# Optimization experiments

Measured on AMD Instinct MI355X. Metric: run time of the kernel, lower is better.

## Reference

```python
import jax, jax.numpy as jnp
import numpy as np
import math


def setup_inputs() -> dict:
    key = jax.random.key(0)
    kq, kk, kv = jax.random.split(key, 3)
    B, H, S, D = 8, 12, 4096, 64
    q = jax.random.normal(kq, (B, H, S, D), dtype=jnp.float32)
    k = jax.random.normal(kk, (B, H, S, D), dtype=jnp.float32)
    v = jax.random.normal(kv, (B, H, S, D), dtype=jnp.float32)
    return {"q": q, "k": k, "v": v}


def reference(q, k, v):
    B, H, S, D = q.shape
    topk = int(2 * math.sqrt(S))  # 128 for S=4096
    # importance = mean + std (torch.std is unbiased -> ddof=1)
    importance = q.mean(axis=-1) + jnp.std(q, axis=-1, ddof=1)  # [B,H,S]
    _, idx = jax.lax.top_k(importance, topk)  # [B,H,topk]
    idx_e = idx[..., None]  # [B,H,topk,1]
    q_s = jnp.take_along_axis(q, idx_e, axis=2)  # [B,H,topk,D]
    k_s = jnp.take_along_axis(k, idx_e, axis=2)
    v_s = jnp.take_along_axis(v, idx_e, axis=2)
    scores = jnp.einsum('bhtd,bhsd->bhts', q_s, k_s) / math.sqrt(D)
    attn = jax.nn.softmax(scores, axis=-1)
    out_s = jnp.einsum('bhts,bhsd->bhtd', attn, v_s)  # [B,H,topk,D]
    # scatter back into a full tensor (torch uses empty_like; we use zeros
    # for the unselected positions so the output is deterministic)
    bI = jnp.arange(B)[:, None, None]
    hI = jnp.arange(H)[None, :, None]
    out = jnp.zeros_like(v).at[bI, hI, idx].set(out_s)  # [B,H,S,D]
    Himg = int(math.sqrt(S))
    return out.reshape(B, -1, Himg, Himg)  # [B, H*D, Himg, Himg]
```

## Files before the change

kernel.cpp:

```cpp
#include <hip/hip_runtime.h>
#include <hip/hip_fp16.h>
#include <math.h>

#define BH_N 96
#define S_N 4096
#define D_N 64
#define TOPK 128

__device__ __forceinline__ unsigned long long orderKey(double d) {
  unsigned long long u = (unsigned long long)__double_as_longlong(d);
  if (u & 0x8000000000000000ULL) u = ~u;
  else u |= 0x8000000000000000ULL;
  return u;
}

__global__ __launch_bounds__(256)
void imp_zero_kernel(const float* __restrict__ q, float* __restrict__ out,
                     double* __restrict__ imp) {
  const int tid = threadIdx.x;
  const size_t off = (size_t)blockIdx.x * 1024 + (size_t)tid * 4;
  const float4 v = *reinterpret_cast<const float4*>(q + off);
  float4 z; z.x = z.y = z.z = z.w = 0.f;
  *reinterpret_cast<float4*>(out + off) = z;

  double s  = (double)v.x + (double)v.y + (double)v.z + (double)v.w;
  double ss = (double)v.x * v.x + (double)v.y * v.y +
              (double)v.z * v.z + (double)v.w * v.w;
#pragma unroll
  for (int m = 1; m < 16; m <<= 1) {
    s  += __shfl_xor(s, m, 64);
    ss += __shfl_xor(ss, m, 64);
  }
  if ((tid & 15) == 0) {
    double mean = s * (1.0 / 64.0);
    double var = (ss - s * s * (1.0 / 64.0)) * (1.0 / 63.0);
    if (var < 0.0) var = 0.0;
    imp[(size_t)blockIdx.x * 16 + (tid >> 4)] = mean + sqrt(var);
  }
}

__global__ __launch_bounds__(256)
void topk_attn_kernel(const float* __restrict__ q, const float* __restrict__ k,
                      const float* __restrict__ v, const double* __restrict__ imp,
                      float* __restrict__ out) {
  __shared__ __align__(16) float sA[8448];
  __shared__ __align__(16) float sB[4160];
  __shared__ int s_idx[TOPK];
  __shared__ int s_red[4];
  __shared__ int s_cnt;

  const int tid = threadIdx.x;
  const int lane = tid & 63;
  const int wv = tid >> 6;
  const int bh = blockIdx.x;
  const double* impb = imp + (size_t)bh * S_N;

  unsigned long long key[16];
#pragma unroll
  for (int i = 0; i < 16; ++i) key[i] = orderKey(impb[i * 256 + tid]);

  unsigned long long lo = 0ULL, hi = ~0ULL;
  while (lo < hi) {
    unsigned long long d = hi - lo;
    unsigned long long mid = lo + (d >> 1) + (d & 1ULL);
    int c = 0;
#pragma unroll
    for (int i = 0; i < 16; ++i) c += (key[i] >= mid) ? 1 : 0;
#pragma unroll
    for (int m = 1; m < 64; m <<= 1) c += __shfl_xor(c, m, 64);
    if (lane == 0) s_red[wv] = c;
    __syncthreads();
    int total = s_red[0] + s_red[1] + s_red[2] + s_red[3];
    __syncthreads();
    if (total >= TOPK) lo = mid; else hi = mid - 1;
  }
  const unsigned long long T = lo;

  if (tid == 0) s_cnt = 0;
  __syncthreads();
#pragma unroll
  for (int i = 0; i < 16; ++i) {
    if (key[i] > T) {
      int slot = atomicAdd(&s_cnt, 1);
      s_idx[slot] = i * 256 + tid;
    }
  }
  __syncthreads();
  const int nsel = s_cnt;
  const int need = TOPK - nsel;
  if (wv == 0 && need > 0) {
    int running = 0;
    for (int base = 0; base < S_N && running < need; base += 64) {
      unsigned long long kk2 = orderKey(impb[base + lane]);
      unsigned long long mask = __ballot(kk2 == T);
      if (kk2 == T) {
        int below = __popcll(mask & ((1ULL << lane) - 1ULL));
        int pos = running + below;
        if (pos < need) s_idx[nsel + pos] = base + lane;
      }
      running += __popcll(mask);
    }
  }
  __syncthreads();

  const size_t baseQ = (size_t)bh * S_N * D_N;
  const int rgrp = tid >> 4;
  const int c4 = (tid & 15) * 4;

#pragma unroll
  for (int it = 0; it < 8; ++it) {
    int r = it * 16 + rgrp;
    int srow = s_idx[r];
    float4 val = *reinterpret_cast<const float4*>(q + baseQ + (size_t)srow * D_N + c4);
    sA[r * 65 + c4 + 0] = val.x;
    sA[r * 65 + c4 + 1] = val.y;
    sA[r * 65 + c4 + 2] = val.z;
    sA[r * 65 + c4 + 3] = val.w;
  }

  float acc[8][8];
#pragma unroll
  for (int j = 0; j < 8; ++j)
#pragma unroll
    for (int m = 0; m < 8; ++m) acc[j][m] = 0.f;

  const int tq = tid >> 4;
  const int sq = tid & 15;

  for (int h = 0; h < 2; ++h) {
    __syncthreads();
#pragma unroll
    for (int it = 0; it < 4; ++it) {
      int r = it * 16 + rgrp;
      int srow = s_idx[h * 64 + r];
      float4 val = *reinterpret_cast<const float4*>(k + baseQ + (size_t)srow * D_N + c4);
      sB[r * 65 + c4 + 0] = val.x;
      sB[r * 65 + c4 + 1] = val.y;
      sB[r * 65 + c4 + 2] = val.z;
      sB[r * 65 + c4 + 3] = val.w;
    }
    __syncthreads();
    for (int kk = 0; kk < 64; ++kk) {
      float qv[8], kv[4];
#pragma unroll
      for (int j = 0; j < 8; ++j) qv[j] = sA[(8 * tq + j) * 65 + kk];
#pragma unroll
      for (int m = 0; m < 4; ++m) kv[m] = sB[(4 * sq + m) * 65 + kk];
#pragma unroll
      for (int j = 0; j < 8; ++j)
#pragma unroll
        for (int m = 0; m < 4; ++m) acc[j][h * 4 + m] += qv[j] * kv[m];
    }
  }
  __syncthreads();

  __half* sP = reinterpret_cast<__half*>(sA);
  float rmax[8], rsum[8];
#pragma unroll
  for (int j = 0; j < 8; ++j) {
    float mx = acc[j][0];
#pragma unroll
    for (int m = 1; m < 8; ++m) mx = fmaxf(mx, acc[j][m]);
    rmax[j] = mx;
  }
#pragma unroll
  for (int mm = 1; mm < 16; mm <<= 1)
#pragma unroll
    for (int j = 0; j < 8; ++j) rmax[j] = fmaxf(rmax[j], __shfl_xor(rmax[j], mm, 64));
#pragma unroll
  for (int j = 0; j < 8; ++j) {
    float sum = 0.f;
#pragma unroll
    for (int m = 0; m < 8; ++m) {
      float p = __expf(0.125f * (acc[j][m] - rmax[j]));
      acc[j][m] = p;
      sum += p;
    }
    rsum[j] = sum;
  }
#pragma unroll
  for (int mm = 1; mm < 16; mm <<= 1)
#pragma unroll
    for (int j = 0; j < 8; ++j) rsum[j] += __shfl_xor(rsum[j], mm, 64);
#pragma unroll
  for (int j = 0; j < 8; ++j) {
    float rinv = 1.f / rsum[j];
#pragma unroll
    for (int h2 = 0; h2 < 2; ++h2)
#pragma unroll
      for (int m = 0; m < 4; ++m) {
        int col = h2 * 64 + 4 * sq + m;
        sP[(8 * tq + j) * 132 + col] = __float2half_rn(acc[j][h2 * 4 + m] * rinv);
      }
  }

  float acc2[8][4];
#pragma unroll
  for (int j = 0; j < 8; ++j)
#pragma unroll
    for (int m = 0; m < 4; ++m) acc2[j][m] = 0.f;

  const int ti = tq, di = sq;
  for (int h = 0; h < 2; ++h) {
    __syncthreads();
#pragma unroll
    for (int it = 0; it < 4; ++it) {
      int r = it * 16 + rgrp;
      int srow = s_idx[h * 64 + r];
      float4 val = *reinterpret_cast<const float4*>(v + baseQ + (size_t)srow * D_N + c4);
      sB[r * 65 + c4 + 0] = val.x;
      sB[r * 65 + c4 + 1] = val.y;
      sB[r * 65 + c4 + 2] = val.z;
      sB[r * 65 + c4 + 3] = val.w;
    }
    __syncthreads();
    for (int s2 = 0; s2 < 64; ++s2) {
      int scol = h * 64 + s2;
      float pj[8], vm[4];
#pragma unroll
      for (int j = 0; j < 8; ++j) pj[j] = __half2float(sP[(8 * ti + j) * 132 + scol]);
#pragma unroll
      for (int m = 0; m < 4; ++m) vm[m] = sB[s2 * 65 + 4 * di + m];
#pragma unroll
      for (int j = 0; j < 8; ++j)
#pragma unroll
        for (int m = 0; m < 4; ++m) acc2[j][m] += pj[j] * vm[m];
    }
  }

#pragma unroll
  for (int j = 0; j < 8; ++j) {
    int row = 8 * ti + j;
    int srow = s_idx[row];
    float4 val;
    val.x = acc2[j][0]; val.y = acc2[j][1]; val.z = acc2[j][2]; val.w = acc2[j][3];
    *reinterpret_cast<float4*>(out + baseQ + (size_t)srow * D_N + 4 * di) = val;
  }
}

extern "C" void kernel_launch(void* const* d_in, const int* in_sizes, int n_in,
                              void* d_out, int out_size, void* d_ws, size_t ws_size,
                              hipStream_t stream) {
  const float* q = (const float*)d_in[0];
  const float* k = (const float*)d_in[1];
  const float* v = (const float*)d_in[2];
  float* out = (float*)d_out;
  double* imp = (double*)d_ws;

  imp_zero_kernel<<<24576, 256, 0, stream>>>(q, out, imp);
  topk_attn_kernel<<<BH_N, 256, 0, stream>>>(q, k, v, imp, out);
}
```

Before: 318.4 us.

## Split top-k selection and attention into separate kernels with more parallelism

```diff
diff --git a/kernel.cpp b/kernel.cpp
--- a/kernel.cpp
+++ b/kernel.cpp
@@ -7,8 +7,10 @@
 #define D_N 64
 #define TOPK 128
 
-__device__ __forceinline__ unsigned long long orderKey(double d) {
-  unsigned long long u = (unsigned long long)__double_as_longlong(d);
+typedef unsigned long long ull;
+
+__device__ __forceinline__ ull orderKey(double d) {
+  ull u = (ull)__double_as_longlong(d);
   if (u & 0x8000000000000000ULL) u = ~u;
   else u |= 0x8000000000000000ULL;
   return u;
@@ -16,7 +18,7 @@
 
 __global__ __launch_bounds__(256)
 void imp_zero_kernel(const float* __restrict__ q, float* __restrict__ out,
-                     double* __restrict__ imp) {
+                     ull* __restrict__ keys) {
   const int tid = threadIdx.x;
   const size_t off = (size_t)blockIdx.x * 1024 + (size_t)tid * 4;
   const float4 v = *reinterpret_cast<const float4*>(q + off);
@@ -35,97 +37,112 @@
     double mean = s * (1.0 / 64.0);
     double var = (ss - s * s * (1.0 / 64.0)) * (1.0 / 63.0);
     if (var < 0.0) var = 0.0;
-    imp[(size_t)blockIdx.x * 16 + (tid >> 4)] = mean + sqrt(var);
-  }
-}
-
-__global__ __launch_bounds__(256)
-void topk_attn_kernel(const float* __restrict__ q, const float* __restrict__ k,
-                      const float* __restrict__ v, const double* __restrict__ imp,
-                      float* __restrict__ out) {
-  __shared__ __align__(16) float sA[8448];
-  __shared__ __align__(16) float sB[4160];
+    keys[(size_t)blockIdx.x * 16 + (tid >> 4)] = orderKey(mean + sqrt(var));
+  }
+}
+
+__global__ __launch_bounds__(1024)
+void sel_kernel(const ull* __restrict__ keys, int* __restrict__ idx_out) {
+  __shared__ int red[2][16];
   __shared__ int s_idx[TOPK];
-  __shared__ int s_red[4];
-  __shared__ int s_cnt;
+  __shared__ int s_tidx[1024];
+  __shared__ int s_cnt, s_tcnt;
 
   const int tid = threadIdx.x;
   const int lane = tid & 63;
   const int wv = tid >> 6;
   const int bh = blockIdx.x;
-  const double* impb = imp + (size_t)bh * S_N;
-
-  unsigned long long key[16];
-#pragma unroll
-  for (int i = 0; i < 16; ++i) key[i] = orderKey(impb[i * 256 + tid]);
-
-  unsigned long long lo = 0ULL, hi = ~0ULL;
+  const ull* kb = keys + (size_t)bh * S_N;
+
+  ull key[4];
+#pragma unroll
+  for (int i = 0; i < 4; ++i) key[i] = kb[i * 1024 + tid];
+
+  if (tid == 0) { s_cnt = 0; s_tcnt = 0; }
+
+  ull lo = 0ULL, hi = ~0ULL;
+  int p = 0;
   while (lo < hi) {
-    unsigned long long d = hi - lo;
-    unsigned long long mid = lo + (d >> 1) + (d & 1ULL);
+    ull d = hi - lo;
+    ull mid = lo + (d >> 1) + (d & 1ULL);
     int c = 0;
 #pragma unroll
-    for (int i = 0; i < 16; ++i) c += (key[i] >= mid) ? 1 : 0;
-#pragma unroll
-    for (int m = 1; m < 64; m <<= 1) c += __shfl_xor(c, m, 64);
-    if (lane == 0) s_red[wv] = c;
-    __syncthreads();
-    int total = s_red[0] + s_red[1] + s_red[2] + s_red[3];
-    __syncthreads();
+    for (int i = 0; i < 4; ++i) c += __popcll(__ballot(key[i] >= mid));
+    if (lane == 0) red[p][wv] = c;
+    __syncthreads();
+    int total = 0;
+#pragma unroll
+    for (int w = 0; w < 16; ++w) total += red[p][w];
     if (total >= TOPK) lo = mid; else hi = mid - 1;
-  }
-  const unsigned long long T = lo;
-
-  if (tid == 0) s_cnt = 0;
-  __syncthreads();
-#pragma unroll
-  for (int i = 0; i < 16; ++i) {
+    p ^= 1;
+  }
+  const ull T = lo;
+
+#pragma unroll
+  for (int i = 0; i < 4; ++i) {
     if (key[i] > T) {
       int slot = atomicAdd(&s_cnt, 1);
-      s_idx[slot] = i * 256 + tid;
+      s_idx[slot] = i * 1024 + tid;
+    } else if (key[i] == T) {
+      int sl = atomicAdd(&s_tcnt, 1);
+      if (sl < 1024) s_tidx[sl] = i * 1024 + tid;
     }
   }
   __syncthreads();
   const int nsel = s_cnt;
   const int need = TOPK - nsel;
   if (wv == 0 && need > 0) {
-    int running = 0;
-    for (int base = 0; base < S_N && running < need; base += 64) {
-      unsigned long long kk2 = orderKey(impb[base + lane]);
-      unsigned long long mask = __ballot(kk2 == T);
-      if (kk2 == T) {
-        int below = __popcll(mask & ((1ULL << lane) - 1ULL));
-        int pos = running + below;
-        if (pos < need) s_idx[nsel + pos] = base + lane;
-      }
-      running += __popcll(mask);
+    int t = s_tcnt < 1024 ? s_tcnt : 1024;
+    for (int sel = 0; sel < need; ++sel) {
+      int mymin = 0x7fffffff;
+      for (int j = lane; j < t; j += 64) mymin = min(mymin, s_tidx[j]);
+#pragma unroll
+      for (int m = 1; m < 64; m <<= 1) mymin = min(mymin, __shfl_xor(mymin, m, 64));
+      if (lane == 0) s_idx[nsel + sel] = mymin;
+      for (int j = lane; j < t; j += 64)
+        if (s_tidx[j] == mymin) s_tidx[j] = 0x7fffffff;
     }
   }
   __syncthreads();
-
-  const size_t baseQ = (size_t)bh * S_N * D_N;
+  if (tid < TOPK) idx_out[bh * TOPK + tid] = s_idx[tid];
+}
+
+__global__ __launch_bounds__(256)
+void attn_kernel(const float* __restrict__ q, const float* __restrict__ k,
+                 const float* __restrict__ v, const int* __restrict__ idx_all,
+                 float* __restrict__ out) {
+  __shared__ __align__(16) float sQ[32 * 65];
+  __shared__ __align__(16) float sB[64 * 65];
+  __shared__ __align__(16) __half sP[32 * 132];
+  __shared__ int s_idx[TOPK];
+
+  const int tid = threadIdx.x;
+  const int bh = blockIdx.x >> 2;
+  const int sub = blockIdx.x & 3;
+  if (tid < TOPK) s_idx[tid] = idx_all[bh * TOPK + tid];
+
+  const size_t base = (size_t)bh * S_N * D_N;
   const int rgrp = tid >> 4;
   const int c4 = (tid & 15) * 4;
-
-#pragma unroll
-  for (int it = 0; it < 8; ++it) {
+  const int rr = tid >> 4;
+  const int cc = tid & 15;
+
+  __syncthreads();
+
+#pragma unroll
+  for (int it = 0; it < 2; ++it) {
     int r = it * 16 + rgrp;
-    int srow = s_idx[r];
-    float4 val = *reinterpret_cast<const float4*>(q + baseQ + (size_t)srow * D_N + c4);
-    sA[r * 65 + c4 + 0] = val.x;
-    sA[r * 65 + c4 + 1] = val.y;
-    sA[r * 65 + c4 + 2] = val.z;
-    sA[r * 65 + c4 + 3] = val.w;
-  }
-
-  float acc[8][8];
-#pragma unroll
-  for (int j = 0; j < 8; ++j)
+    int srow = s_idx[sub * 32 + r];
+    float4 val = *reinterpret_cast<const float4*>(q + base + (size_t)srow * D_N + c4);
+    sQ[r * 65 + c4 + 0] = val.x; sQ[r * 65 + c4 + 1] = val.y;
+    sQ[r * 65 + c4 + 2] = val.z; sQ[r * 65 + c4 + 3] = val.w;
+  }
+
+  float acc[2][8];
+#pragma unroll
+  for (int j = 0; j < 2; ++j)
 #pragma unroll
     for (int m = 0; m < 8; ++m) acc[j][m] = 0.f;
-
-  const int tq = tid >> 4;
-  const int sq = tid & 15;
 
   for (int h = 0; h < 2; ++h) {
     __syncthreads();
@@ -133,31 +150,31 @@
     for (int it = 0; it < 4; ++it) {
       int r = it * 16 + rgrp;
       int srow = s_idx[h * 64 + r];
-      float4 val = *reinterpret_cast<const float4*>(k + baseQ + (size_t)srow * D_N + c4);
-      sB[r * 65 + c4 + 0] = val.x;
-      sB[r * 65 + c4 + 1] = val.y;
-      sB[r * 65 + c4 + 2] = val.z;
-      sB[r * 65 + c4 + 3] = val.w;
-    }
-    __syncthreads();
-    for (int kk = 0; kk < 64; ++kk) {
-      float qv[8], kv[4];
-#pragma unroll
-      for (int j = 0; j < 8; ++j) qv[j] = sA[(8 * tq + j) * 65 + kk];
-#pragma unroll
-      for (int m = 0; m < 4; ++m) kv[m] = sB[(4 * sq + m) * 65 + kk];
-#pragma unroll
-      for (int j = 0; j < 8; ++j)
-#pragma unroll
-        for (int m = 0; m < 4; ++m) acc[j][h * 4 + m] += qv[j] * kv[m];
-    }
-  }
-  __syncthreads();
-
-  __half* sP = reinterpret_cast<__half*>(sA);
-  float rmax[8], rsum[8];
-#pragma unroll
-  for (int j = 0; j < 8; ++j) {
+      float4 val = *reinterpret_cast<const float4*>(k + base + (size_t)srow * D_N + c4);
+      sB[r * 65 + c4 + 0] = val.x; sB[r * 65 + c4 + 1] = val.y;
+      sB[r * 65 + c4 + 2] = val.z; sB[r * 65 + c4 + 3] = val.w;
+    }
+    __syncthreads();
+    for (int kk = 0; kk < 64; kk += 2) {
+#pragma unroll
+      for (int u = 0; u < 2; ++u) {
+        float qv0 = sQ[(2 * rr + 0) * 65 + kk + u];
+        float qv1 = sQ[(2 * rr + 1) * 65 + kk + u];
+        float kv[4];
+#pragma unroll
+        for (int m = 0; m < 4; ++m) kv[m] = sB[(cc * 4 + m) * 65 + kk + u];
+#pragma unroll
+        for (int m = 0; m < 4; ++m) {
+          acc[0][h * 4 + m] += qv0 * kv[m];
+          acc[1][h * 4 + m] += qv1 * kv[m];
+        }
+      }
+    }
+  }
+
+  float rmax[2], rsum[2];
+#pragma unroll
+  for (int j = 0; j < 2; ++j) {
     float mx = acc[j][0];
 #pragma unroll
     for (int m = 1; m < 8; ++m) mx = fmaxf(mx, acc[j][m]);
@@ -166,75 +183,72 @@
 #pragma unroll
   for (int mm = 1; mm < 16; mm <<= 1)
 #pragma unroll
-    for (int j = 0; j < 8; ++j) rmax[j] = fmaxf(rmax[j], __shfl_xor(rmax[j], mm, 64));
-#pragma unroll
-  for (int j = 0; j < 8; ++j) {
+    for (int j = 0; j < 2; ++j) rmax[j] = fmaxf(rmax[j], __shfl_xor(rmax[j], mm, 64));
+#pragma unroll
+  for (int j = 0; j < 2; ++j) {
     float sum = 0.f;
 #pragma unroll
     for (int m = 0; m < 8; ++m) {
-      float p = __expf(0.125f * (acc[j][m] - rmax[j]));
-      acc[j][m] = p;
-      sum += p;
+      float pe = __expf(0.125f * (acc[j][m] - rmax[j]));
+      acc[j][m] = pe;
+      sum += pe;
     }
     rsum[j] = sum;
   }
 #pragma unroll
   for (int mm = 1; mm < 16; mm <<= 1)
 #pragma unroll
-    for (int j = 0; j < 8; ++j) rsum[j] += __shfl_xor(rsum[j], mm, 64);
-#pragma unroll
-  for (int j = 0; j < 8; ++j) {
+    for (int j = 0; j < 2; ++j) rsum[j] += __shfl_xor(rsum[j], mm, 64);
+#pragma unroll
+  for (int j = 0; j < 2; ++j) {
     float rinv = 1.f / rsum[j];
 #pragma unroll
     for (int h2 = 0; h2 < 2; ++h2)
 #pragma unroll
       for (int m = 0; m < 4; ++m) {
-        int col = h2 * 64 + 4 * sq + m;
-        sP[(8 * tq + j) * 132 + col] = __float2half_rn(acc[j][h2 * 4 + m] * rinv);
+        int col = h2 * 64 + cc * 4 + m;
+        sP[(2 * rr + j) * 132 + col] = __float2half_rn(acc[j][h2 * 4 + m] * rinv);
       }
   }
 
-  float acc2[8][4];
-#pragma unroll
-  for (int j = 0; j < 8; ++j)
+  float acc2[2][4];
+#pragma unroll
+  for (int j = 0; j < 2; ++j)
 #pragma unroll
     for (int m = 0; m < 4; ++m) acc2[j][m] = 0.f;
 
-  const int ti = tq, di = sq;
   for (int h = 0; h < 2; ++h) {
     __syncthreads();
 #pragma unroll
     for (int it = 0; it < 4; ++it) {
       int r = it * 16 + rgrp;
       int srow = s_idx[h * 64 + r];
-      float4 val = *reinterpret_cast<const float4*>(v + baseQ + (size_t)srow * D_N + c4);
-      sB[r * 65 + c4 + 0] = val.x;
-      sB[r * 65 + c4 + 1] = val.y;
-      sB[r * 65 + c4 + 2] = val.z;
-      sB[r * 65 + c4 + 3] = val.w;
+      float4 val = *reinterpret_cast<const float4*>(v + base + (size_t)srow * D_N + c4);
+      sB[r * 65 + c4 + 0] = val.x; sB[r * 65 + c4 + 1] = val.y;
+      sB[r * 65 + c4 + 2] = val.z; sB[r * 65 + c4 + 3] = val.w;
     }
     __syncthreads();
     for (int s2 = 0; s2 < 64; ++s2) {
       int scol = h * 64 + s2;
-      float pj[8], vm[4];
-#pragma unroll
-      for (int j = 0; j < 8; ++j) pj[j] = __half2float(sP[(8 * ti + j) * 132 + scol]);
-#pragma unroll
-      for (int m = 0; m < 4; ++m) vm[m] = sB[s2 * 65 + 4 * di + m];
-#pragma unroll
-      for (int j = 0; j < 8; ++j)
-#pragma unroll
-        for (int m = 0; m < 4; ++m) acc2[j][m] += pj[j] * vm[m];
-    }
-  }
-
-#pragma unroll
-  for (int j = 0; j < 8; ++j) {
-    int row = 8 * ti + j;
-    int srow = s_idx[row];
+      float pj0 = __half2float(sP[(2 * rr + 0) * 132 + scol]);
+      float pj1 = __half2float(sP[(2 * rr + 1) * 132 + scol]);
+      float vm[4];
+#pragma unroll
+      for (int m = 0; m < 4; ++m) vm[m] = sB[s2 * 65 + cc * 4 + m];
+#pragma unroll
+      for (int m = 0; m < 4; ++m) {
+        acc2[0][m] += pj0 * vm[m];
+        acc2[1][m] += pj1 * vm[m];
+      }
+    }
+  }
+
+#pragma unroll
+  for (int j = 0; j < 2; ++j) {
+    int srow = s_idx[sub * 32 + 2 * rr + j];
     float4 val;
     val.x = acc2[j][0]; val.y = acc2[j][1]; val.z = acc2[j][2]; val.w = acc2[j][3];
-    *reinterpret_cast<float4*>(out + baseQ + (size_t)srow * D_N + 4 * di) = val;
+    *reinterpret_cast<float4*>(out + base + (size_t)srow * D_N + cc * 4) = val;
   }
 }
 
@@ -245,8 +259,10 @@
   const float* k = (const float*)d_in[1];
   const float* v = (const float*)d_in[2];
   float* out = (float*)d_out;
-  double* imp = (double*)d_ws;
-
-  imp_zero_kernel<<<24576, 256, 0, stream>>>(q, out, imp);
-  topk_attn_kernel<<<BH_N, 256, 0, stream>>>(q, k, v, imp, out);
-}
+  ull* keys = (ull*)d_ws;
+  int* idx = (int*)((char*)d_ws + (size_t)BH_N * S_N * 8);
+
+  imp_zero_kernel<<<24576, 256, 0, stream>>>(q, out, keys);
+  sel_kernel<<<BH_N, 1024, 0, stream>>>(keys, idx);
+  attn_kernel<<<BH_N * 4, 256, 0, stream>>>(q, k, v, idx, out);
+}
```

Result: faster. 307.8 us (-3.3%).
